# Kernel optimization log

Hardware: AMD Instinct MI355X
Metric: run time of the kernel (lower is better)

Reference implementation:

```python
import jax, jax.numpy as jnp
import numpy as np
from jax import lax
import math

S, V, D, L, B = 64, 50257, 586, 4, 32  # seq_len, num_tokens, num_inputs, num_layers, batch_size
K1 = S // 4 + 1   # 17, conv1 kernel
P1 = S // 16 + 1  # 5,  avgpool1 kernel
P2 = S // 32 + 1  # 3,  avgpool2 kernel
EPS = 1e-5


def setup_inputs() -> dict:
    key = jax.random.key(0)
    ks = jax.random.split(key, 14)
    tokens = jax.random.randint(ks[0], (S, B), 0, V)
    emb = jax.random.normal(ks[1], (V, D - 3), jnp.float32) * 0.02
    # pos_embeds = randn(S,1,3).repeat(1,B,1)
    pos = jnp.tile(jax.random.normal(ks[2], (S, 1, 3), jnp.float32), (1, B, 1))
    gamma = 1.0 + 0.1 * jax.random.normal(ks[3], (L, S), jnp.float32)
    beta = 0.1 * jax.random.normal(ks[4], (L, S), jnp.float32)
    w1 = jax.random.normal(ks[5], (B // 2, B, K1), jnp.float32) * 0.02
    b1 = jax.random.normal(ks[6], (B // 2,), jnp.float32) * 0.02
    w2 = jax.random.normal(ks[7], (B // 4, B // 2, 1), jnp.float32) * 0.02
    b2 = jax.random.normal(ks[8], (B // 4,), jnp.float32) * 0.02
    w3 = jax.random.normal(ks[9], (B, B // 4, 3), jnp.float32) * 0.02
    b3 = jax.random.normal(ks[10], (B,), jnp.float32) * 0.02
    wl = jax.random.normal(ks[11], (128, 36), jnp.float32) * 0.1
    bl = jax.random.normal(ks[12], (128,), jnp.float32) * 0.1
    return {"tokens": tokens, "emb": emb, "pos": pos, "gamma": gamma, "beta": beta,
            "w1": w1, "b1": b1, "w2": w2, "b2": b2, "w3": w3, "b3": b3,
            "wl": wl, "bl": bl}


def _conv1d(x, w, b):
    # x: (N, C_in, Lx), w: (C_out, C_in, K)
    y = lax.conv_general_dilated(x, w, (1,), 'VALID',
                                 dimension_numbers=('NCH', 'OIH', 'NCH'))
    return y + b[None, :, None]


def _avgpool1d(x, k):
    # torch AvgPool1d: stride=kernel, floor mode
    n, c, lx = x.shape
    lo = lx // k
    return x[:, :, :lo * k].reshape(n, c, lo, k).mean(axis=-1)


def _logits(tokens, emb, pos, gamma, beta, w1, b1, w2, b2, w3, b3, wl, bl):
    x = emb[tokens] * math.sqrt(D)          # (S, B, D-3)
    x = jnp.concatenate([x, pos], axis=2)   # (S, B, D)
    for l in range(L):
        xb = x.swapaxes(0, 1)               # (B, S, D): BatchNorm1d over channels=S
        mean = xb.mean(axis=(0, 2), keepdims=True)
        var = xb.var(axis=(0, 2), keepdims=True)  # biased, training-mode batch stats
        xb = gamma[l][None, :, None] * (xb - mean) * lax.rsqrt(var + EPS) + beta[l][None, :, None]
        x = xb.swapaxes(0, 1)
    out = _conv1d(x, w1, b1)                # (S, B/2, D-16) = (64, 16, 570)
    out = _avgpool1d(out, P1)               # (64, 16, 114)
    out = _conv1d(out, w2, b2)              # (64, 8, 114)
    out = _avgpool1d(out, P2)               # (64, 8, 38)
    out = _conv1d(out, w3, b3)              # (64, 32, 36)
    out = jnp.einsum('sbk,vk->sbv', out, wl) + bl  # (64, 32, 128)
    return out


def reference(tokens, emb, pos, gamma, beta, w1, b1, w2, b2, w3, b3, wl, bl):
    out = _logits(tokens, emb, pos, gamma, beta, w1, b1, w2, b2, w3, b3, wl, bl)
    # vectorized replacement for the triple-nested .item() argmax loop
    return jnp.argmax(out, axis=-1).astype(jnp.float32)  # (S, B)
```

## Files before the change

kernel.cpp:

```cpp
#include <hip/hip_runtime.h>
#include <math.h>

#define SS 64
#define BB 32
#define DD 586
#define DE 583
#define U1 114
#define U2 38
#define T3 36
#define NTOK 18752
#define NSTAT (SS*BB)
#define SQD 24.207436873820409f


__global__ __launch_bounds__(256) void k_main(
    const int* __restrict__ tokens, const float* __restrict__ emb,
    const float* __restrict__ pos, const float* __restrict__ w1,
    double* __restrict__ rowsumd, double* __restrict__ rowsqd,
    float* __restrict__ part)
{
  const int s = blockIdx.x, g = blockIdx.y;
  const int tid = threadIdx.x;
  __shared__ float xs[8*DD];
  __shared__ int stok[8];
  if (tid < 8) stok[tid] = tokens[s*BB + g*8 + tid];
  __syncthreads();
  {
    const int rr = tid >> 5, l = tid & 31;
    const float* row = emb + (size_t)stok[rr]*DE;
    double sum = 0.0, sq = 0.0;
    #pragma unroll
    for (int j = 0; j < 19; ++j) {
      int d = l + 32*j;
      if (d < DD) {
        float v = (d < DE) ? row[d] * SQD
                           : pos[(s*BB + g*8 + rr)*3 + (d - DE)];
        xs[rr*DD + d] = v;
        sum += v; sq += (double)v*v;
      }
    }
    for (int off = 16; off > 0; off >>= 1) {
      sum += __shfl_down(sum, off, 32);
      sq  += __shfl_down(sq, off, 32);
    }
    if (l == 0) {
      rowsumd[s*BB + g*8 + rr] = sum;
      rowsqd [s*BB + g*8 + rr] = sq;
    }
  }
  __syncthreads();
  const int up = tid & 127;
  const int oh = __builtin_amdgcn_readfirstlane(tid >> 7);
  const int u  = (up < U1) ? up : (U1 - 1);
  float acc[8] = {0,0,0,0,0,0,0,0};
  for (int cc = 0; cc < 8; ++cc) {
    const float* xr = &xs[cc*DD + 5*u];
    float xv[21];
    #pragma unroll
    for (int m = 0; m < 21; ++m) xv[m] = xr[m];
    float xw[17];
    #pragma unroll
    for (int k = 0; k < 17; ++k)
      xw[k] = ((xv[k] + xv[k+1]) + (xv[k+2] + xv[k+3])) + xv[k+4];
    #pragma unroll
    for (int j = 0; j < 8; ++j) {
      const float* wj = w1 + ((size_t)(oh*8 + j)*BB + (g*8 + cc))*17;
      float a = 0.f;
      #pragma unroll
      for (int k = 0; k < 17; ++k) a += xw[k] * wj[k];
      acc[j] += a;
    }
  }
  if (up < U1) {
    float* pb = part + ((size_t)(g*SS + s)*16 + oh*8)*U1 + up;
    #pragma unroll
    for (int j = 0; j < 8; ++j) pb[j*U1] = acc[j] * 0.2f;
  }
}

__global__ __launch_bounds__(256) void k_tail(
    const double* __restrict__ rowsumd, const double* __restrict__ rowsqd,
    const float* __restrict__ gamma, const float* __restrict__ beta,
    const float* __restrict__ part, const float* __restrict__ w1,
    const float* __restrict__ b1, const float* __restrict__ w2,
    const float* __restrict__ b2, const float* __restrict__ w3,
    const float* __restrict__ b3, const float* __restrict__ wl,
    const float* __restrict__ bl, float* __restrict__ out)
{
  const int s = blockIdx.x, tid = threadIdx.x;
  __shared__ float o2[16*U1];
  __shared__ float p2[16*U2];
  __shared__ float o4[8*U2];
  __shared__ float o5[32*T3];
  __shared__ float wlb[128*37];
  __shared__ float blb[128];
  __shared__ float wsumb[16];
  __shared__ float sAl, sDe;
  for (int idx = tid; idx < 128*36; idx += 256) {
    int v = idx / 36, t = idx - v*36;
    wlb[v*37 + t] = wl[idx];
  }
  if (tid < 128) blb[tid] = bl[tid];
  {
    const int o = tid >> 4, i = tid & 15;
    float acc = 0.f;
    for (int j = i; j < BB*17; j += 16) acc += w1[o*BB*17 + j];
    for (int off = 8; off > 0; off >>= 1) acc += __shfl_down(acc, off, 16);
    if (i == 0) wsumb[o] = acc;
  }
  if (tid < 32) {
    double sm = rowsumd[s*BB + tid], qq = rowsqd[s*BB + tid];
    for (int off = 16; off > 0; off >>= 1) {
      sm += __shfl_down(sm, off, 32);
      qq += __shfl_down(qq, off, 32);
    }
    if (tid == 0) {
      double m0d = sm / (double)NTOK;
      float m0 = (float)m0d;
      float v0 = (float)(qq / (double)NTOK - m0d*m0d);
      float a = 1.0f;
      for (int l = 0; l < 4; ++l) {
        float r = 1.0f / sqrtf(a*a*v0 + 1e-5f);
        a = gamma[l*SS + s] * r * a;
      }
      sAl = a;
      sDe = beta[3*SS + s] - a*m0;
    }
  }
  __syncthreads();
  const float al = sAl, de = sDe;
  for (int idx = tid; idx < 16*U1; idx += 256) {
    int o = idx / U1;
    float psum = part[(size_t)(0*SS + s)*16*U1 + idx]
               + part[(size_t)(1*SS + s)*16*U1 + idx]
               + part[(size_t)(2*SS + s)*16*U1 + idx]
               + part[(size_t)(3*SS + s)*16*U1 + idx];
    o2[idx] = al*psum + de*wsumb[o] + b1[o];
  }
  __syncthreads();
  for (int i2 = tid; i2 < 16*U2; i2 += 256) {
    int o = i2 / U2, v = i2 - o*U2;
    p2[i2] = (o2[o*U1 + 3*v] + o2[o*U1 + 3*v+1] + o2[o*U1 + 3*v+2]) * (1.f/3.f);
  }
  __syncthreads();
  for (int i2 = tid; i2 < 8*U2; i2 += 256) {
    int p = i2 / U2, v = i2 - p*U2;
    float acc = b2[p];
    #pragma unroll
    for (int o = 0; o < 16; ++o) acc += p2[o*U2 + v] * w2[p*16 + o];
    o4[i2] = acc;
  }
  __syncthreads();
  for (int i2 = tid; i2 < 32*T3; i2 += 256) {
    int q = i2 / T3, t = i2 - q*T3;
    float acc = b3[q];
    #pragma unroll
    for (int p = 0; p < 8; ++p) {
      acc += o4[p*U2 + t    ] * w3[(q*8+p)*3 + 0]
           + o4[p*U2 + t + 1] * w3[(q*8+p)*3 + 1]
           + o4[p*U2 + t + 2] * w3[(q*8+p)*3 + 2];
    }
    o5[i2] = acc;
  }
  __syncthreads();
  const int q = tid >> 3, vs = tid & 7;
  float best = -1e30f; int bidx = 0;
  const float* orow = &o5[q*T3];
  for (int i = 0; i < 16; ++i) {
    int v = vs + 8*i;
    float acc = blb[v];
    const float* wr = &wlb[v*37];
    #pragma unroll
    for (int t = 0; t < 36; ++t) acc += orow[t] * wr[t];
    if (acc > best) { best = acc; bidx = v; }
  }
  #pragma unroll
  for (int off = 1; off < 8; off <<= 1) {
    float ov = __shfl_xor(best, off);
    int oi = __shfl_xor(bidx, off);
    if (ov > best || (ov == best && oi < bidx)) { best = ov; bidx = oi; }
  }
  if (vs == 0) out[s*BB + q] = (float)bidx;
}

extern "C" void kernel_launch(void* const* d_in, const int* in_sizes, int n_in,
                              void* d_out, int out_size, void* d_ws, size_t ws_size,
                              hipStream_t stream)
{
  const int*   tokens = (const int*)  d_in[0];
  const float* emb    = (const float*)d_in[1];
  const float* pos    = (const float*)d_in[2];
  const float* gamma  = (const float*)d_in[3];
  const float* beta   = (const float*)d_in[4];
  const float* w1     = (const float*)d_in[5];
  const float* b1     = (const float*)d_in[6];
  const float* w2     = (const float*)d_in[7];
  const float* b2     = (const float*)d_in[8];
  const float* w3     = (const float*)d_in[9];
  const float* b3     = (const float*)d_in[10];
  const float* wl     = (const float*)d_in[11];
  const float* bl     = (const float*)d_in[12];
  float* out = (float*)d_out;

  double* rowsumd = (double*)d_ws;
  double* rowsqd  = rowsumd + NSTAT;
  float*  part    = (float*)(rowsqd + NSTAT);

  k_main<<<dim3(SS, 4), dim3(256), 0, stream>>>(
      tokens, emb, pos, w1, rowsumd, rowsqd, part);
  k_tail<<<dim3(SS), dim3(256), 0, stream>>>(
      rowsumd, rowsqd, gamma, beta, part, w1, b1, w2, b2, w3, b3,
      wl, bl, out);
}
```

Baseline: 196.1 us.

## Fuse embedding, conv1 and tail into a single per-sequence-position kernel

Merges the two kernels into one launch with one block per sequence position. Each block gathers all 32 embedding rows into shared memory, computes the batch-norm row statistics locally, runs the full conv1 over all 32 input channels, then continues with the existing tail. This removes the second launch and the global-memory round trip for the row statistics and conv1 partial sums. In exchange the grid shrinks from 256 to 64 blocks, leaving most CUs idle, while each block does four times the conv work and uses far more shared memory.

```diff
diff --git a/kernel.cpp b/kernel.cpp
--- a/kernel.cpp
+++ b/kernel.cpp
@@ -9,85 +9,20 @@
 #define U2 38
 #define T3 36
 #define NTOK 18752
-#define NSTAT (SS*BB)
 #define SQD 24.207436873820409f
 
-
-__global__ __launch_bounds__(256) void k_main(
+__global__ __launch_bounds__(256) void k_fused(
     const int* __restrict__ tokens, const float* __restrict__ emb,
-    const float* __restrict__ pos, const float* __restrict__ w1,
-    double* __restrict__ rowsumd, double* __restrict__ rowsqd,
-    float* __restrict__ part)
-{
-  const int s = blockIdx.x, g = blockIdx.y;
-  const int tid = threadIdx.x;
-  __shared__ float xs[8*DD];
-  __shared__ int stok[8];
-  if (tid < 8) stok[tid] = tokens[s*BB + g*8 + tid];
-  __syncthreads();
-  {
-    const int rr = tid >> 5, l = tid & 31;
-    const float* row = emb + (size_t)stok[rr]*DE;
-    double sum = 0.0, sq = 0.0;
-    #pragma unroll
-    for (int j = 0; j < 19; ++j) {
-      int d = l + 32*j;
-      if (d < DD) {
-        float v = (d < DE) ? row[d] * SQD
-                           : pos[(s*BB + g*8 + rr)*3 + (d - DE)];
-        xs[rr*DD + d] = v;
-        sum += v; sq += (double)v*v;
-      }
-    }
-    for (int off = 16; off > 0; off >>= 1) {
-      sum += __shfl_down(sum, off, 32);
-      sq  += __shfl_down(sq, off, 32);
-    }
-    if (l == 0) {
-      rowsumd[s*BB + g*8 + rr] = sum;
-      rowsqd [s*BB + g*8 + rr] = sq;
-    }
-  }
-  __syncthreads();
-  const int up = tid & 127;
-  const int oh = __builtin_amdgcn_readfirstlane(tid >> 7);
-  const int u  = (up < U1) ? up : (U1 - 1);
-  float acc[8] = {0,0,0,0,0,0,0,0};
-  for (int cc = 0; cc < 8; ++cc) {
-    const float* xr = &xs[cc*DD + 5*u];
-    float xv[21];
-    #pragma unroll
-    for (int m = 0; m < 21; ++m) xv[m] = xr[m];
-    float xw[17];
-    #pragma unroll
-    for (int k = 0; k < 17; ++k)
-      xw[k] = ((xv[k] + xv[k+1]) + (xv[k+2] + xv[k+3])) + xv[k+4];
-    #pragma unroll
-    for (int j = 0; j < 8; ++j) {
-      const float* wj = w1 + ((size_t)(oh*8 + j)*BB + (g*8 + cc))*17;
-      float a = 0.f;
-      #pragma unroll
-      for (int k = 0; k < 17; ++k) a += xw[k] * wj[k];
-      acc[j] += a;
-    }
-  }
-  if (up < U1) {
-    float* pb = part + ((size_t)(g*SS + s)*16 + oh*8)*U1 + up;
-    #pragma unroll
-    for (int j = 0; j < 8; ++j) pb[j*U1] = acc[j] * 0.2f;
-  }
-}
-
-__global__ __launch_bounds__(256) void k_tail(
-    const double* __restrict__ rowsumd, const double* __restrict__ rowsqd,
-    const float* __restrict__ gamma, const float* __restrict__ beta,
-    const float* __restrict__ part, const float* __restrict__ w1,
+    const float* __restrict__ pos, const float* __restrict__ gamma,
+    const float* __restrict__ beta, const float* __restrict__ w1,
     const float* __restrict__ b1, const float* __restrict__ w2,
     const float* __restrict__ b2, const float* __restrict__ w3,
     const float* __restrict__ b3, const float* __restrict__ wl,
     const float* __restrict__ bl, float* __restrict__ out)
 {
-  const int s = blockIdx.x, tid = threadIdx.x;
+  const int s = blockIdx.x;
+  const int tid = threadIdx.x;
+  __shared__ float xs[BB*DD];
   __shared__ float o2[16*U1];
   __shared__ float p2[16*U2];
   __shared__ float o4[8*U2];
@@ -96,6 +31,10 @@
   __shared__ float blb[128];
   __shared__ float wsumb[16];
   __shared__ float sAl, sDe;
+  __shared__ double rs[BB], rq[BB];
+  __shared__ int stok[BB];
+
+  if (tid < BB) stok[tid] = tokens[s*BB + tid];
   for (int idx = tid; idx < 128*36; idx += 256) {
     int v = idx / 36, t = idx - v*36;
     wlb[v*37 + t] = wl[idx];
@@ -108,8 +47,35 @@
     for (int off = 8; off > 0; off >>= 1) acc += __shfl_down(acc, off, 16);
     if (i == 0) wsumb[o] = acc;
   }
+  __syncthreads();
+
+  {
+    const int rr0 = tid >> 5, l = tid & 31;
+    for (int it = 0; it < 4; ++it) {
+      const int rr = rr0 + 8*it;
+      const float* row = emb + (size_t)stok[rr]*DE;
+      double sum = 0.0, sq = 0.0;
+      #pragma unroll
+      for (int j = 0; j < 19; ++j) {
+        int d = l + 32*j;
+        if (d < DD) {
+          float v = (d < DE) ? row[d] * SQD
+                             : pos[(s*BB + rr)*3 + (d - DE)];
+          xs[rr*DD + d] = v;
+          sum += v; sq += (double)v*v;
+        }
+      }
+      for (int off = 16; off > 0; off >>= 1) {
+        sum += __shfl_down(sum, off, 32);
+        sq  += __shfl_down(sq, off, 32);
+      }
+      if (l == 0) { rs[rr] = sum; rq[rr] = sq; }
+    }
+  }
+  __syncthreads();
+
   if (tid < 32) {
-    double sm = rowsumd[s*BB + tid], qq = rowsqd[s*BB + tid];
+    double sm = rs[tid], qq = rq[tid];
     for (int off = 16; off > 0; off >>= 1) {
       sm += __shfl_down(sm, off, 32);
       qq += __shfl_down(qq, off, 32);
@@ -119,9 +85,9 @@
       float m0 = (float)m0d;
       float v0 = (float)(qq / (double)NTOK - m0d*m0d);
       float a = 1.0f;
-      for (int l = 0; l < 4; ++l) {
+      for (int l2 = 0; l2 < 4; ++l2) {
         float r = 1.0f / sqrtf(a*a*v0 + 1e-5f);
-        a = gamma[l*SS + s] * r * a;
+        a = gamma[l2*SS + s] * r * a;
       }
       sAl = a;
       sDe = beta[3*SS + s] - a*m0;
@@ -129,15 +95,40 @@
   }
   __syncthreads();
   const float al = sAl, de = sDe;
-  for (int idx = tid; idx < 16*U1; idx += 256) {
-    int o = idx / U1;
-    float psum = part[(size_t)(0*SS + s)*16*U1 + idx]
-               + part[(size_t)(1*SS + s)*16*U1 + idx]
-               + part[(size_t)(2*SS + s)*16*U1 + idx]
-               + part[(size_t)(3*SS + s)*16*U1 + idx];
-    o2[idx] = al*psum + de*wsumb[o] + b1[o];
-  }
-  __syncthreads();
+
+  {
+    const int up = tid & 127;
+    const int oh = __builtin_amdgcn_readfirstlane(tid >> 7);
+    const int u  = (up < U1) ? up : (U1 - 1);
+    float acc[8] = {0,0,0,0,0,0,0,0};
+    for (int cc = 0; cc < BB; ++cc) {
+      const float* xr = &xs[cc*DD + 5*u];
+      float xv[21];
+      #pragma unroll
+      for (int m = 0; m < 21; ++m) xv[m] = xr[m];
+      float xw[17];
+      #pragma unroll
+      for (int k = 0; k < 17; ++k)
+        xw[k] = ((xv[k] + xv[k+1]) + (xv[k+2] + xv[k+3])) + xv[k+4];
+      #pragma unroll
+      for (int j = 0; j < 8; ++j) {
+        const float* wj = w1 + ((size_t)(oh*8 + j)*BB + cc)*17;
+        float a = 0.f;
+        #pragma unroll
+        for (int k = 0; k < 17; ++k) a += xw[k] * wj[k];
+        acc[j] += a;
+      }
+    }
+    if (up < U1) {
+      #pragma unroll
+      for (int j = 0; j < 8; ++j) {
+        int o = oh*8 + j;
+        o2[o*U1 + up] = al*(acc[j]*0.2f) + de*wsumb[o] + b1[o];
+      }
+    }
+  }
+  __syncthreads();
+
   for (int i2 = tid; i2 < 16*U2; i2 += 256) {
     int o = i2 / U2, v = i2 - o*U2;
     p2[i2] = (o2[o*U1 + 3*v] + o2[o*U1 + 3*v+1] + o2[o*U1 + 3*v+2]) * (1.f/3.f);
@@ -163,6 +154,7 @@
     o5[i2] = acc;
   }
   __syncthreads();
+
   const int q = tid >> 3, vs = tid & 7;
   float best = -1e30f; int bidx = 0;
   const float* orow = &o5[q*T3];
@@ -201,14 +193,8 @@
   const float* wl     = (const float*)d_in[11];
   const float* bl     = (const float*)d_in[12];
   float* out = (float*)d_out;
-
-  double* rowsumd = (double*)d_ws;
-  double* rowsqd  = rowsumd + NSTAT;
-  float*  part    = (float*)(rowsqd + NSTAT);
-
-  k_main<<<dim3(SS, 4), dim3(256), 0, stream>>>(
-      tokens, emb, pos, w1, rowsumd, rowsqd, part);
-  k_tail<<<dim3(SS), dim3(256), 0, stream>>>(
-      rowsumd, rowsqd, gamma, beta, part, w1, b1, w2, b2, w3, b3,
-      wl, bl, out);
+  (void)d_ws; (void)ws_size;
+
+  k_fused<<<dim3(SS), dim3(256), 0, stream>>>(
+      tokens, emb, pos, gamma, beta, w1, b1, w2, b2, w3, b3, wl, bl, out);
 }
```

After: 211.8 us. 1.08x slower.
